# Kernel optimization log

Measured on AMD Instinct MI355X. Metric: run time of the kernel, lower is better.

## Reference

```python
import jax, jax.numpy as jnp
import numpy as np

N = 20000       # nodes
E = 320000      # edges (before self-loops)
F_IN = 1024     # num_features
H = 4           # head_num
C = 64          # hidden_size
NC = 4          # n_classes
NEG_SLOPE = 0.2 # PyG GATConv default


def setup_inputs() -> dict:
    key = jax.random.key(0)
    ks = jax.random.split(key, 16)
    def w(k, shape, fan_in):
        return jax.random.normal(k, shape, dtype=jnp.float32) / np.sqrt(fan_in)
    x = jax.random.normal(ks[0], (N, F_IN), dtype=jnp.float32)
    edge_index = jax.random.randint(ks[1], (2, E), 0, N, dtype=jnp.int64)
    return {
        "x": x,
        "edge_index": edge_index,
        # layer 1: F_IN -> H*C, concat
        "w1": w(ks[2], (F_IN, H * C), F_IN),
        "as1": w(ks[3], (H, C), C),
        "ad1": w(ks[4], (H, C), C),
        "b1": jnp.zeros((H * C,), jnp.float32),
        # layer 2: H*C -> H*C, concat
        "w2": w(ks[5], (H * C, H * C), H * C),
        "as2": w(ks[6], (H, C), C),
        "ad2": w(ks[7], (H, C), C),
        "b2": jnp.zeros((H * C,), jnp.float32),
        # out layer: H*C -> C, 1 head, concat=False
        "w3": w(ks[8], (H * C, 1 * C), H * C),
        "as3": w(ks[9], (1, C), C),
        "ad3": w(ks[10], (1, C), C),
        "b3": jnp.zeros((C,), jnp.float32),
        # classifier
        "wc": w(ks[11], (C, NC), C),
        "bc": jnp.zeros((NC,), jnp.float32),
    }


def gat_layer(x, src, dst, W, a_src, a_dst, bias, concat):
    """PyG GATConv (eval mode, self-loops already added to src/dst)."""
    n = x.shape[0]
    Hh, Cc = a_src.shape
    h = (x @ W).reshape(n, Hh, Cc)                       # [N,H,C]
    al_s = jnp.sum(h * a_src[None], axis=-1)             # [N,H]
    al_d = jnp.sum(h * a_dst[None], axis=-1)             # [N,H]
    e = al_s[src] + al_d[dst]                            # [E,H]
    e = jax.nn.leaky_relu(e, NEG_SLOPE)
    # segment softmax over incoming edges of each destination node
    emax = jax.ops.segment_max(e, dst, num_segments=n)   # [N,H]
    ex = jnp.exp(e - emax[dst])
    denom = jax.ops.segment_sum(ex, dst, num_segments=n) # [N,H]
    alpha = ex / (denom[dst] + 1e-16)                    # [E,H]
    msg = h[src] * alpha[..., None]                      # [E,H,C]
    out = jax.ops.segment_sum(msg, dst, num_segments=n)  # [N,H,C]
    if concat:
        out = out.reshape(n, Hh * Cc)
    else:
        out = out.mean(axis=1)
    return out + bias


def reference(x, edge_index, w1, as1, ad1, b1, w2, as2, ad2, b2,
              w3, as3, ad3, b3, wc, bc):
    n = x.shape[0]
    loop = jnp.arange(n, dtype=edge_index.dtype)
    src = jnp.concatenate([edge_index[0], loop])
    dst = jnp.concatenate([edge_index[1], loop])
    out = jax.nn.relu(gat_layer(x, src, dst, w1, as1, ad1, b1, True))
    out = jax.nn.relu(gat_layer(out, src, dst, w2, as2, ad2, b2, True))
    out = gat_layer(out, src, dst, w3, as3, ad3, b3, False)
    return out @ wc + bc                                  # [N, n_classes]
```

## Files before the change

### kernel.cpp

```cpp
#include <hip/hip_runtime.h>

#define N_NODES 20000
#define N_EDGES 320000
#define ET (N_EDGES + N_NODES)
#define F_IN 1024
#define HC 256
#define NC 4

typedef unsigned short ushort_t;
typedef __attribute__((ext_vector_type(8))) short short8;
typedef __attribute__((ext_vector_type(4))) float f32x4;

__device__ inline ushort_t f2bf(float f) {
    unsigned u = __float_as_uint(f);
    unsigned r = (u + 0x7fffu + ((u >> 16) & 1u)) >> 16;
    return (ushort_t)r;
}
__device__ inline float bf2f(ushort_t u) {
    return __uint_as_float(((unsigned)u) << 16);
}

__device__ inline unsigned cvt_pk_bf16(float lo, float hi) {
    unsigned r;
    asm("v_cvt_pk_bf16_f32 %0, %1, %2" : "=v"(r) : "v"(lo), "v"(hi));
    return r;
}

#define GLOAD16(gp, lp) __builtin_amdgcn_global_load_lds( \
    (const __attribute__((address_space(1))) void*)(gp),  \
    (__attribute__((address_space(3))) void*)(lp), 16, 0, 0)

__global__ void count_kernel(const int* __restrict__ ei, int* __restrict__ counts) {
    int e = blockIdx.x * blockDim.x + threadIdx.x;
    if (e >= ET) return;
    int dst = (e < N_EDGES) ? ei[N_EDGES + e] : (e - N_EDGES);
    atomicAdd(&counts[dst], 1);
}

__global__ void scan_kernel(const int* __restrict__ counts, int* __restrict__ row_ptr,
                            int* __restrict__ cursor) {
    __shared__ int sums[1024];
    int t = threadIdx.x;
    const int per = (N_NODES + 1023) / 1024;
    int b = t * per;
    int e = min(b + per, N_NODES);
    int s = 0;
    for (int i = b; i < e; ++i) s += counts[i];
    sums[t] = s;
    __syncthreads();
    for (int off = 1; off < 1024; off <<= 1) {
        int v = (t >= off) ? sums[t - off] : 0;
        __syncthreads();
        sums[t] += v;
        __syncthreads();
    }
    int run = (t == 0) ? 0 : sums[t - 1];
    for (int i = b; i < e; ++i) {
        row_ptr[i] = run;
        cursor[i]  = run;
        run += counts[i];
    }
    if (t == 0) row_ptr[N_NODES] = ET;
}

__global__ void scatter_kernel(const int* __restrict__ ei, int* __restrict__ cursor,
                               int* __restrict__ col) {
    int e = blockIdx.x * blockDim.x + threadIdx.x;
    if (e >= ET) return;
    int src, dst;
    if (e < N_EDGES) { src = ei[e]; dst = ei[N_EDGES + e]; }
    else             { src = dst = e - N_EDGES; }
    int pos = atomicAdd(&cursor[dst], 1);
    col[pos] = src;
}

__global__ void split_T(const float* __restrict__ in, ushort_t* __restrict__ hi,
                        ushort_t* __restrict__ lo, int K, int Nn) {
    int idx = blockIdx.x * blockDim.x + threadIdx.x;
    if (idx >= K * Nn) return;
    int k = idx / Nn, n = idx - k * Nn;
    float v = in[idx];
    ushort_t h = f2bf(v);
    hi[(size_t)n * K + k] = h;
    lo[(size_t)n * K + k] = f2bf(v - bf2f(h));
}

#define AL_EPILOGUE()                                                              \
    {                                                                              \
        float asv[NF], adv[NF];                                                    \
        _Pragma("unroll")                                                          \
        for (int j = 0; j < NF; ++j) {                                             \
            int col = bn + wn * SN + j * 16 + (lane & 15);                         \
            asv[j] = as_w[col];                                                    \
            adv[j] = ad_w[col];                                                    \
        }                                                                          \
        float* s_as = (float*)smem;                                   \
        float* s_ad = (float*)smem + 2 * BM;                                       \
        _Pragma("unroll")                                                          \
        for (int i = 0; i < MF; ++i) {                                             \
            _Pragma("unroll")                                                      \
            for (int rr = 0; rr < 4; ++rr) {                                       \
                float ps = 0.f, pd = 0.f;                                          \
                _Pragma("unroll")                                                  \
                for (int j = 0; j < NF; ++j) {                                     \
                    ps += acc[i][j][rr] * asv[j];                                  \
                    pd += acc[i][j][rr] * adv[j];                                  \
                }                                                                  \
                _Pragma("unroll")                                                  \
                for (int o = 1; o < 16; o <<= 1) {                                 \
                    ps += __shfl_xor(ps, o, 64);                                   \
                    pd += __shfl_xor(pd, o, 64);                                   \
                }                                                                  \
                if ((lane & 15) == 0) {                                            \
                    int rl = wm * SM + i * 16 + (lane >> 4) * 4 + rr;              \
                    s_as[wn * BM + rl] = ps;                                       \
                    s_ad[wn * BM + rl] = pd;                                       \
                }                                                                  \
            }                                                                      \
        }                                                                          \
        __syncthreads();                                                           \
        if (t < BM) {                                                              \
            int row = bm + t;                                                      \
            if (row < M) {                                                         \
                int hb = bn >> 6;                                                  \
                als[row * H + hb] = s_as[t] + s_as[BM + t];                        \
                ald[row * H + hb] = s_ad[t] + s_ad[BM + t];                        \
            }                                                                      \
        }                                                                          \
    }

template<int GY, int H>
__launch_bounds__(256)
__global__ void gemm_f32a(const float* __restrict__ X,
                          const ushort_t* __restrict__ BTh, const ushort_t* __restrict__ BTl,
                          float* __restrict__ C, const float* __restrict__ as_w,
                          const float* __restrict__ ad_w, float* __restrict__ als,
                          float* __restrict__ ald, int M, int K, int NT) {
    constexpr int BM = 128, BN = 64, SM = 64, SN = 32, MF = 4, NF = 2;
    __shared__ __align__(16) char smem[24576];
    char* Ash = smem;
    char* Asl = smem + 8192;
    char* Bsh = smem + 16384;
    char* Bsl = smem + 20480;

    const int t = threadIdx.x, lane = t & 63, w = t >> 6;
    const int wm = w >> 1, wn = w & 1;
    const int nwg = gridDim.x;
    const int id = blockIdx.x;
    const int q = nwg >> 3, r = nwg & 7;
    const int xcd = id & 7, idx = id >> 3;
    const int logical = (xcd < r ? xcd * (q + 1) : r * (q + 1) + (xcd - r) * q) + idx;
    const int bm = (logical / GY) * BM, bn = (logical % GY) * BN;

    const int achk = lane & 3;
    const float* xRow[2]; int aoff[2];
    #pragma unroll
    for (int qq = 0; qq < 2; ++qq) {
        int arow = (w * 2 + qq) * 16 + (lane >> 2);
        int grow = min(bm + arow, M - 1);
        xRow[qq] = X + (size_t)grow * K + achk * 8;
        aoff[qq] = arow * 64 + ((achk ^ ((arow >> 1) & 3)) * 16);
    }
    const int gchunk = ((lane & 3) ^ ((lane >> 3) & 3)) * 16;
    const int brow = w * 16 + (lane >> 2);
    const size_t gB = (size_t)(bn + brow) * K * 2 + gchunk;
    const int lB = w * 1024;

    const char* Bhb = (const char*)BTh;
    const char* Blb = (const char*)BTl;
    const int c16 = (lane >> 4);

    f32x4 acc[MF][NF];
    #pragma unroll
    for (int i = 0; i < MF; ++i)
        #pragma unroll
        for (int j = 0; j < NF; ++j) acc[i][j] = (f32x4){0.f, 0.f, 0.f, 0.f};

    float4 c0[2], c1[2];
    #pragma unroll
    for (int qq = 0; qq < 2; ++qq) {
        c0[qq] = *(const float4*)(xRow[qq]);
        c1[qq] = *(const float4*)(xRow[qq] + 4);
    }

    for (int k0 = 0; k0 < K; k0 += 32) {
        float4 n0[2], n1[2];
        if (k0 + 32 < K) {
            #pragma unroll
            for (int qq = 0; qq < 2; ++qq) {
                n0[qq] = *(const float4*)(xRow[qq] + k0 + 32);
                n1[qq] = *(const float4*)(xRow[qq] + k0 + 36);
            }
        }
        #pragma unroll
        for (int qq = 0; qq < 2; ++qq) {
            float vv[8] = {c0[qq].x, c0[qq].y, c0[qq].z, c0[qq].w,
                           c1[qq].x, c1[qq].y, c1[qq].z, c1[qq].w};
            unsigned hp[4], lp[4];
            #pragma unroll
            for (int j = 0; j < 4; ++j) {
                unsigned h = cvt_pk_bf16(vv[2 * j], vv[2 * j + 1]);
                float h0 = __uint_as_float(h << 16);
                float h1 = __uint_as_float(h & 0xFFFF0000u);
                hp[j] = h;
                lp[j] = cvt_pk_bf16(vv[2 * j] - h0, vv[2 * j + 1] - h1);
            }
            *(uint4*)(Ash + aoff[qq]) = make_uint4(hp[0], hp[1], hp[2], hp[3]);
            *(uint4*)(Asl + aoff[qq]) = make_uint4(lp[0], lp[1], lp[2], lp[3]);
        }
        size_t kb = (size_t)k0 * 2;
        GLOAD16(Bhb + gB + kb, Bsh + lB);
        GLOAD16(Blb + gB + kb, Bsl + lB);
        __syncthreads();
        short8 afh[MF], afl[MF], bfh[NF], bfl[NF];
        #pragma unroll
        for (int i = 0; i < MF; ++i) {
            int row = wm * SM + i * 16 + (lane & 15);
            int off = row * 64 + ((c16 ^ ((row >> 1) & 3)) * 16);
            afh[i] = *(const short8*)(Ash + off);
            afl[i] = *(const short8*)(Asl + off);
        }
        #pragma unroll
        for (int j = 0; j < NF; ++j) {
            int row = wn * SN + j * 16 + (lane & 15);
            int off = row * 64 + ((c16 ^ ((row >> 1) & 3)) * 16);
            bfh[j] = *(const short8*)(Bsh + off);
            bfl[j] = *(const short8*)(Bsl + off);
        }
        #pragma unroll
        for (int i = 0; i < MF; ++i)
            #pragma unroll
            for (int j = 0; j < NF; ++j) {
                acc[i][j] = __builtin_amdgcn_mfma_f32_16x16x32_bf16(afh[i], bfh[j], acc[i][j], 0, 0, 0);
                acc[i][j] = __builtin_amdgcn_mfma_f32_16x16x32_bf16(afh[i], bfl[j], acc[i][j], 0, 0, 0);
                acc[i][j] = __builtin_amdgcn_mfma_f32_16x16x32_bf16(afl[i], bfh[j], acc[i][j], 0, 0, 0);
            }
        __syncthreads();
        #pragma unroll
        for (int qq = 0; qq < 2; ++qq) { c0[qq] = n0[qq]; c1[qq] = n1[qq]; }
    }
    #pragma unroll
    for (int i = 0; i < MF; ++i) {
        int rbase = bm + wm * SM + i * 16 + (lane >> 4) * 4;
        #pragma unroll
        for (int j = 0; j < NF; ++j) {
            int col = bn + wn * SN + j * 16 + (lane & 15);
            #pragma unroll
            for (int rr = 0; rr < 4; ++rr)
                if (rbase + rr < M) C[(size_t)(rbase + rr) * NT + col] = acc[i][j][rr];
        }
    }
    AL_EPILOGUE()
}

template<int GY, int H>
__launch_bounds__(256)
__global__ void gemm_mfma(const ushort_t* __restrict__ Ah, const ushort_t* __restrict__ Al,
                          const ushort_t* __restrict__ BTh, const ushort_t* __restrict__ BTl,
                          float* __restrict__ C, const float* __restrict__ as_w,
                          const float* __restrict__ ad_w, float* __restrict__ als,
                          float* __restrict__ ald, int M, int K, int NT) {
    constexpr int BM = 128, BN = 64, SM = 64, SN = 32, MF = 4, NF = 2;
    __shared__ __align__(16) char smem[24576];
    char* Ash = smem;
    char* Asl = smem + 8192;
    char* Bsh = smem + 16384;
    char* Bsl = smem + 20480;

    const int t = threadIdx.x, lane = t & 63, w = t >> 6;
    const int wm = w >> 1, wn = w & 1;
    const int nwg = gridDim.x;
    const int id = blockIdx.x;
    const int q = nwg >> 3, r = nwg & 7;
    const int xcd = id & 7, idx = id >> 3;
    const int logical = (xcd < r ? xcd * (q + 1) : r * (q + 1) + (xcd - r) * q) + idx;
    const int bm = (logical / GY) * BM, bn = (logical % GY) * BN;
    const int gchunk = ((lane & 3) ^ ((lane >> 3) & 3)) * 16;

    size_t gA[2]; int lA[2];
    #pragma unroll
    for (int qq = 0; qq < 2; ++qq) {
        int arow = (w * 2 + qq) * 16 + (lane >> 2);
        int grow = min(bm + arow, M - 1);
        gA[qq] = (size_t)grow * K * 2 + gchunk;
        lA[qq] = (w * 2 + qq) * 1024;
    }
    const int brow = w * 16 + (lane >> 2);
    const size_t gB = (size_t)(bn + brow) * K * 2 + gchunk;
    const int lB = w * 1024;

    const char* Ahb = (const char*)Ah;
    const char* Alb = (const char*)Al;
    const char* Bhb = (const char*)BTh;
    const char* Blb = (const char*)BTl;
    const int c16 = (lane >> 4);

    f32x4 acc[MF][NF];
    #pragma unroll
    for (int i = 0; i < MF; ++i)
        #pragma unroll
        for (int j = 0; j < NF; ++j) acc[i][j] = (f32x4){0.f, 0.f, 0.f, 0.f};

    for (int k0 = 0; k0 < K; k0 += 32) {
        size_t kb = (size_t)k0 * 2;
        #pragma unroll
        for (int qq = 0; qq < 2; ++qq) {
            GLOAD16(Ahb + gA[qq] + kb, Ash + lA[qq]);
            GLOAD16(Alb + gA[qq] + kb, Asl + lA[qq]);
        }
        GLOAD16(Bhb + gB + kb, Bsh + lB);
        GLOAD16(Blb + gB + kb, Bsl + lB);
        __syncthreads();
        short8 afh[MF], afl[MF], bfh[NF], bfl[NF];
        #pragma unroll
        for (int i = 0; i < MF; ++i) {
            int row = wm * SM + i * 16 + (lane & 15);
            int off = row * 64 + ((c16 ^ ((row >> 1) & 3)) * 16);
            afh[i] = *(const short8*)(Ash + off);
            afl[i] = *(const short8*)(Asl + off);
        }
        #pragma unroll
        for (int j = 0; j < NF; ++j) {
            int row = wn * SN + j * 16 + (lane & 15);
            int off = row * 64 + ((c16 ^ ((row >> 1) & 3)) * 16);
            bfh[j] = *(const short8*)(Bsh + off);
            bfl[j] = *(const short8*)(Bsl + off);
        }
        #pragma unroll
        for (int i = 0; i < MF; ++i)
            #pragma unroll
            for (int j = 0; j < NF; ++j) {
                acc[i][j] = __builtin_amdgcn_mfma_f32_16x16x32_bf16(afh[i], bfh[j], acc[i][j], 0, 0, 0);
                acc[i][j] = __builtin_amdgcn_mfma_f32_16x16x32_bf16(afh[i], bfl[j], acc[i][j], 0, 0, 0);
                acc[i][j] = __builtin_amdgcn_mfma_f32_16x16x32_bf16(afl[i], bfh[j], acc[i][j], 0, 0, 0);
            }
        __syncthreads();
    }
    #pragma unroll
    for (int i = 0; i < MF; ++i) {
        int rbase = bm + wm * SM + i * 16 + (lane >> 4) * 4;
        #pragma unroll
        for (int j = 0; j < NF; ++j) {
            int col = bn + wn * SN + j * 16 + (lane & 15);
            #pragma unroll
            for (int rr = 0; rr < 4; ++rr)
                if (rbase + rr < M) C[(size_t)(rbase + rr) * NT + col] = acc[i][j][rr];
        }
    }
    AL_EPILOGUE()
}

template<int H>
__launch_bounds__(256)
__global__ void alpha_kernel(const float* __restrict__ als, const float* __restrict__ ald,
                             const int* __restrict__ row_ptr, const int* __restrict__ col,
                             float* __restrict__ alpha) {
    int lane = threadIdx.x & 63, w = threadIdx.x >> 6;
    int dst = blockIdx.x * 4 + w;
    if (dst >= N_NODES) return;
    int beg = row_ptr[dst], deg = row_ptr[dst + 1] - beg;
    constexpr int ES = 64 / H;
    int i_loc = lane / H, hh = lane % H;
    float ad = ald[dst * H + hh];
    float m = -1e30f, den = 0.f;
    for (int base = 0; base < deg; base += ES) {
        int i = base + i_loc;
        if (i < deg) {
            float e = als[col[beg + i] * H + hh] + ad;
            e = (e > 0.f) ? e : 0.2f * e;
            float nm = fmaxf(m, e);
            den = den * __expf(m - nm) + __expf(e - nm);
            m = nm;
        }
    }
    #pragma unroll
    for (int off = H; off < 64; off <<= 1) {
        float mo = __shfl_xor(m, off, 64);
        float dn = __shfl_xor(den, off, 64);
        float nm = fmaxf(m, mo);
        den = den * __expf(m - nm) + dn * __expf(mo - nm);
        m = nm;
    }
    float rden = 1.f / (den + 1e-16f);
    for (int base = 0; base < deg; base += ES) {
        int i = base + i_loc;
        if (i < deg) {
            float e = als[col[beg + i] * H + hh] + ad;
            e = (e > 0.f) ? e : 0.2f * e;
            alpha[(size_t)hh * ET + beg + i] = __expf(e - m) * rden;
        }
    }
}

template<int CT, int CW, int H, bool RELU, bool SPLIT>
__launch_bounds__(256)
__global__ void agg_v3(const float* __restrict__ h, const float* __restrict__ alpha,
                       const int* __restrict__ row_ptr, const int* __restrict__ col,
                       const float* __restrict__ bias,
                       ushort_t* __restrict__ oh, ushort_t* __restrict__ ol,
                       float* __restrict__ of) {
    constexpr int NS  = CT / CW;
    constexpr int LPT = CW / 4;
    constexpr int TPW = 64 / LPT;
    static_assert(NS == H, "slice==head mapping");
    __shared__ int   s_src[4][64];
    __shared__ float s_alp[4][64];
    const int nwg = gridDim.x;
    const int q = nwg >> 3;
    int id = blockIdx.x;
    int logical = (id & 7) * q + (id >> 3);
    int slice = logical / (N_NODES / 4);
    int g = logical - slice * (N_NODES / 4);
    int lane = threadIdx.x & 63, w = threadIdx.x >> 6;
    int dst = g * 4 + w;
    int beg = row_ptr[dst], deg = row_ptr[dst + 1] - beg;
    int team = lane / LPT;
    int cc = (lane & (LPT - 1)) * 4;

    const int*   colP = col + beg;
    const float* aP   = alpha + (size_t)slice * ET + beg;
    const float* hS   = h + slice * CW + cc;

    float4 acc = make_float4(0.f, 0.f, 0.f, 0.f);
    for (int base = 0; base < deg; base += 64) {
        int cnt = min(64, deg - base);
        if (lane < cnt) {
            s_src[w][lane] = colP[base + lane];
            s_alp[w][lane] = aP[base + lane];
        }
        for (int i = team; i < cnt; i += TPW) {
            int   s = s_src[w][i];
            float a = s_alp[w][i];
            float4 hv = *(const float4*)&hS[s * CT];
            acc.x += a * hv.x; acc.y += a * hv.y;
            acc.z += a * hv.z; acc.w += a * hv.w;
        }
    }
    #pragma unroll
    for (int off = LPT; off < 64; off <<= 1) {
        acc.x += __shfl_xor(acc.x, off, 64);
        acc.y += __shfl_xor(acc.y, off, 64);
        acc.z += __shfl_xor(acc.z, off, 64);
        acc.w += __shfl_xor(acc.w, off, 64);
    }
    if (team == 0) {
        int ch = slice * CW + cc;
        float4 bv = *(const float4*)&bias[ch];
        float v0 = acc.x + bv.x, v1 = acc.y + bv.y, v2 = acc.z + bv.z, v3 = acc.w + bv.w;
        if (RELU) {
            v0 = fmaxf(v0, 0.f); v1 = fmaxf(v1, 0.f);
            v2 = fmaxf(v2, 0.f); v3 = fmaxf(v3, 0.f);
        }
        size_t idx = (size_t)dst * CT + ch;
        if (SPLIT) {
            ushort4 h4, l4;
            h4.x = f2bf(v0); l4.x = f2bf(v0 - bf2f(h4.x));
            h4.y = f2bf(v1); l4.y = f2bf(v1 - bf2f(h4.y));
            h4.z = f2bf(v2); l4.z = f2bf(v2 - bf2f(h4.z));
            h4.w = f2bf(v3); l4.w = f2bf(v3 - bf2f(h4.w));
            *(ushort4*)&oh[idx] = h4;
            *(ushort4*)&ol[idx] = l4;
        } else {
            *(float4*)&of[idx] = make_float4(v0, v1, v2, v3);
        }
    }
}

__global__ void classifier_kernel(const float* __restrict__ x, const float* __restrict__ wc,
                                  const float* __restrict__ bc, float* __restrict__ out) {
    int n = blockIdx.x * blockDim.x + threadIdx.x;
    if (n >= N_NODES) return;
    float acc[NC] = {bc[0], bc[1], bc[2], bc[3]};
    for (int c = 0; c < 64; ++c) {
        float xv = x[(size_t)n * 64 + c];
        #pragma unroll
        for (int k = 0; k < NC; ++k) acc[k] += xv * wc[c * NC + k];
    }
    #pragma unroll
    for (int k = 0; k < NC; ++k) out[(size_t)n * NC + k] = acc[k];
}

extern "C" void kernel_launch(void* const* d_in, const int* in_sizes, int n_in,
                              void* d_out, int out_size, void* d_ws, size_t ws_size,
                              hipStream_t stream) {
    const float* x   = (const float*)d_in[0];
    const int*   ei  = (const int*)d_in[1];
    const float* w1  = (const float*)d_in[2];
    const float* as1 = (const float*)d_in[3];
    const float* ad1 = (const float*)d_in[4];
    const float* b1  = (const float*)d_in[5];
    const float* w2  = (const float*)d_in[6];
    const float* as2 = (const float*)d_in[7];
    const float* ad2 = (const float*)d_in[8];
    const float* b2  = (const float*)d_in[9];
    const float* w3  = (const float*)d_in[10];
    const float* as3 = (const float*)d_in[11];
    const float* ad3 = (const float*)d_in[12];
    const float* b3  = (const float*)d_in[13];
    const float* wc  = (const float*)d_in[14];
    const float* bc  = (const float*)d_in[15];
    float* out = (float*)d_out;

    char* ws = (char*)d_ws;
    size_t off = 0;
    auto alloc = [&](size_t bytes) -> char* {
        char* p = ws + off;
        off = (off + bytes + 255) & ~(size_t)255;
        return p;
    };

    int* counts  = (int*)alloc(N_NODES * 4);
    int* cursor  = (int*)alloc(N_NODES * 4);
    int* row_ptr = (int*)alloc((N_NODES + 1) * 4);
    int* colidx  = (int*)alloc(ET * 4);
    float* als   = (float*)alloc(N_NODES * 4 * 4);
    float* ald   = (float*)alloc(N_NODES * 4 * 4);
    float* alpha = (float*)alloc((size_t)4 * ET * 4);
    float* B0    = (float*)alloc((size_t)N_NODES * HC * 4);

    ushort_t* w1Th = (ushort_t*)alloc((size_t)F_IN * HC * 2);
    ushort_t* w1Tl = (ushort_t*)alloc((size_t)F_IN * HC * 2);
    ushort_t* w2Th = (ushort_t*)alloc((size_t)HC * HC * 2);
    ushort_t* w2Tl = (ushort_t*)alloc((size_t)HC * HC * 2);
    ushort_t* w3Th = (ushort_t*)alloc((size_t)HC * 64 * 2);
    ushort_t* w3Tl = (ushort_t*)alloc((size_t)HC * 64 * 2);
    ushort_t* B1h  = (ushort_t*)alloc((size_t)N_NODES * HC * 2);
    ushort_t* B1l  = (ushort_t*)alloc((size_t)N_NODES * HC * 2);
    float*    B1f  = (float*)alloc((size_t)N_NODES * 64 * 4);

    hipMemsetAsync(counts, 0, N_NODES * sizeof(int), stream);
    int eb = (ET + 255) / 256;
    count_kernel<<<eb, 256, 0, stream>>>(ei, counts);
    scan_kernel<<<1, 1024, 0, stream>>>(counts, row_ptr, cursor);
    scatter_kernel<<<eb, 256, 0, stream>>>(ei, cursor, colidx);

    split_T<<<(F_IN * HC + 255) / 256, 256, 0, stream>>>(w1, w1Th, w1Tl, F_IN, HC);
    split_T<<<(HC * HC + 255) / 256, 256, 0, stream>>>(w2, w2Th, w2Tl, HC, HC);
    split_T<<<(HC * 64 + 255) / 256, 256, 0, stream>>>(w3, w3Th, w3Tl, HC, 64);

    const int nwg128 = ((N_NODES + 127) / 128) * (HC / 64);
    const int nblk_dst = N_NODES / 4;
    gemm_f32a<4, 4><<<nwg128, 256, 0, stream>>>(x, w1Th, w1Tl, B0, as1, ad1, als, ald,
                                                N_NODES, F_IN, HC);
    alpha_kernel<4><<<nblk_dst, 256, 0, stream>>>(als, ald, row_ptr, colidx, alpha);
    agg_v3<256, 64, 4, true, true><<<4 * nblk_dst, 256, 0, stream>>>(
        B0, alpha, row_ptr, colidx, b1, B1h, B1l, nullptr);
    gemm_mfma<4, 4><<<nwg128, 256, 0, stream>>>(B1h, B1l, w2Th, w2Tl, B0, as2, ad2, als, ald,
                                                N_NODES, HC, HC);
    alpha_kernel<4><<<nblk_dst, 256, 0, stream>>>(als, ald, row_ptr, colidx, alpha);
    agg_v3<256, 64, 4, true, true><<<4 * nblk_dst, 256, 0, stream>>>(
        B0, alpha, row_ptr, colidx, b2, B1h, B1l, nullptr);
    const int nwg3 = (N_NODES + 127) / 128;
    gemm_mfma<1, 1><<<nwg3, 256, 0, stream>>>(B1h, B1l, w3Th, w3Tl, B0, as3, ad3, als, ald,
                                              N_NODES, HC, 64);
    alpha_kernel<1><<<nblk_dst, 256, 0, stream>>>(als, ald, row_ptr, colidx, alpha);
    agg_v3<64, 64, 1, false, false><<<nblk_dst, 256, 0, stream>>>(
        B0, alpha, row_ptr, colidx, b3, nullptr, nullptr, B1f);
    classifier_kernel<<<(N_NODES + 255) / 256, 256, 0, stream>>>(B1f, wc, bc, out);
}
```

Baseline: 298.9 us.

## Double K-step per barrier in GEMMs and shrink layer-3 tile to 64 rows

Both GEMM kernels now stage 64 K-elements per iteration (two 32-wide sub-tiles) before a single pair of barriers, halving the number of syncthreads per K sweep. The layer-3 GEMM is templated on BM and launched with 64-row tiles so more workgroups cover the 20000 rows. This doubles LDS use per block (48KB for the main GEMMs), which may reduce occupancy, and assumes K is a multiple of 64.

New measurement: 292.2 us. -2.2%, faster.

```diff
diff --git a/kernel.cpp b/kernel.cpp
--- a/kernel.cpp
+++ b/kernel.cpp
@@ -137,11 +137,7 @@
                           const float* __restrict__ ad_w, float* __restrict__ als,
                           float* __restrict__ ald, int M, int K, int NT) {
     constexpr int BM = 128, BN = 64, SM = 64, SN = 32, MF = 4, NF = 2;
-    __shared__ __align__(16) char smem[24576];
-    char* Ash = smem;
-    char* Asl = smem + 8192;
-    char* Bsh = smem + 16384;
-    char* Bsl = smem + 20480;
+    __shared__ __align__(16) char smem[49152];
 
     const int t = threadIdx.x, lane = t & 63, w = t >> 6;
     const int wm = w >> 1, wn = w & 1;
@@ -169,6 +165,7 @@
     const char* Bhb = (const char*)BTh;
     const char* Blb = (const char*)BTl;
     const int c16 = (lane >> 4);
+    const int NTs = K / 64;
 
     f32x4 acc[MF][NF];
     #pragma unroll
@@ -176,68 +173,81 @@
         #pragma unroll
         for (int j = 0; j < NF; ++j) acc[i][j] = (f32x4){0.f, 0.f, 0.f, 0.f};
 
-    float4 c0[2], c1[2];
-    #pragma unroll
-    for (int qq = 0; qq < 2; ++qq) {
-        c0[qq] = *(const float4*)(xRow[qq]);
-        c1[qq] = *(const float4*)(xRow[qq] + 4);
-    }
-
-    for (int k0 = 0; k0 < K; k0 += 32) {
-        float4 n0[2], n1[2];
-        if (k0 + 32 < K) {
-            #pragma unroll
-            for (int qq = 0; qq < 2; ++qq) {
-                n0[qq] = *(const float4*)(xRow[qq] + k0 + 32);
-                n1[qq] = *(const float4*)(xRow[qq] + k0 + 36);
-            }
-        }
-        #pragma unroll
-        for (int qq = 0; qq < 2; ++qq) {
-            float vv[8] = {c0[qq].x, c0[qq].y, c0[qq].z, c0[qq].w,
-                           c1[qq].x, c1[qq].y, c1[qq].z, c1[qq].w};
-            unsigned hp[4], lp[4];
-            #pragma unroll
-            for (int j = 0; j < 4; ++j) {
-                unsigned h = cvt_pk_bf16(vv[2 * j], vv[2 * j + 1]);
-                float h0 = __uint_as_float(h << 16);
-                float h1 = __uint_as_float(h & 0xFFFF0000u);
-                hp[j] = h;
-                lp[j] = cvt_pk_bf16(vv[2 * j] - h0, vv[2 * j + 1] - h1);
-            }
-            *(uint4*)(Ash + aoff[qq]) = make_uint4(hp[0], hp[1], hp[2], hp[3]);
-            *(uint4*)(Asl + aoff[qq]) = make_uint4(lp[0], lp[1], lp[2], lp[3]);
-        }
-        size_t kb = (size_t)k0 * 2;
-        GLOAD16(Bhb + gB + kb, Bsh + lB);
-        GLOAD16(Blb + gB + kb, Bsl + lB);
-        __syncthreads();
-        short8 afh[MF], afl[MF], bfh[NF], bfl[NF];
-        #pragma unroll
-        for (int i = 0; i < MF; ++i) {
-            int row = wm * SM + i * 16 + (lane & 15);
-            int off = row * 64 + ((c16 ^ ((row >> 1) & 3)) * 16);
-            afh[i] = *(const short8*)(Ash + off);
-            afl[i] = *(const short8*)(Asl + off);
-        }
-        #pragma unroll
-        for (int j = 0; j < NF; ++j) {
-            int row = wn * SN + j * 16 + (lane & 15);
-            int off = row * 64 + ((c16 ^ ((row >> 1) & 3)) * 16);
-            bfh[j] = *(const short8*)(Bsh + off);
-            bfl[j] = *(const short8*)(Bsl + off);
-        }
-        #pragma unroll
-        for (int i = 0; i < MF; ++i)
-            #pragma unroll
-            for (int j = 0; j < NF; ++j) {
-                acc[i][j] = __builtin_amdgcn_mfma_f32_16x16x32_bf16(afh[i], bfh[j], acc[i][j], 0, 0, 0);
-                acc[i][j] = __builtin_amdgcn_mfma_f32_16x16x32_bf16(afh[i], bfl[j], acc[i][j], 0, 0, 0);
-                acc[i][j] = __builtin_amdgcn_mfma_f32_16x16x32_bf16(afl[i], bfh[j], acc[i][j], 0, 0, 0);
+    float4 cur0[2][2], cur1[2][2], nxt0[2][2], nxt1[2][2];
+    #pragma unroll
+    for (int qq = 0; qq < 2; ++qq)
+        #pragma unroll
+        for (int kc = 0; kc < 2; ++kc) {
+            cur0[qq][kc] = *(const float4*)(xRow[qq] + kc * 32);
+            cur1[qq][kc] = *(const float4*)(xRow[qq] + kc * 32 + 4);
+        }
+
+    for (int ts = 0; ts < NTs; ++ts) {
+        size_t kb = (size_t)ts * 128;
+        #pragma unroll
+        for (int kc = 0; kc < 2; ++kc) {
+            GLOAD16(Bhb + gB + kb + kc * 64, smem + 32768 + kc * 4096 + lB);
+            GLOAD16(Blb + gB + kb + kc * 64, smem + 40960 + kc * 4096 + lB);
+        }
+        if (ts + 1 < NTs) {
+            #pragma unroll
+            for (int qq = 0; qq < 2; ++qq)
+                #pragma unroll
+                for (int kc = 0; kc < 2; ++kc) {
+                    nxt0[qq][kc] = *(const float4*)(xRow[qq] + (ts + 1) * 64 + kc * 32);
+                    nxt1[qq][kc] = *(const float4*)(xRow[qq] + (ts + 1) * 64 + kc * 32 + 4);
+                }
+        }
+        #pragma unroll
+        for (int qq = 0; qq < 2; ++qq)
+            #pragma unroll
+            for (int kc = 0; kc < 2; ++kc) {
+                float vv[8] = {cur0[qq][kc].x, cur0[qq][kc].y, cur0[qq][kc].z, cur0[qq][kc].w,
+                               cur1[qq][kc].x, cur1[qq][kc].y, cur1[qq][kc].z, cur1[qq][kc].w};
+                unsigned hp[4], lp[4];
+                #pragma unroll
+                for (int j = 0; j < 4; ++j) {
+                    unsigned h = cvt_pk_bf16(vv[2 * j], vv[2 * j + 1]);
+                    float h0 = __uint_as_float(h << 16);
+                    float h1 = __uint_as_float(h & 0xFFFF0000u);
+                    hp[j] = h;
+                    lp[j] = cvt_pk_bf16(vv[2 * j] - h0, vv[2 * j + 1] - h1);
+                }
+                *(uint4*)(smem + kc * 8192 + aoff[qq])         = make_uint4(hp[0], hp[1], hp[2], hp[3]);
+                *(uint4*)(smem + 16384 + kc * 8192 + aoff[qq]) = make_uint4(lp[0], lp[1], lp[2], lp[3]);
             }
         __syncthreads();
         #pragma unroll
-        for (int qq = 0; qq < 2; ++qq) { c0[qq] = n0[qq]; c1[qq] = n1[qq]; }
+        for (int kc = 0; kc < 2; ++kc) {
+            short8 afh[MF], afl[MF], bfh[NF], bfl[NF];
+            #pragma unroll
+            for (int i = 0; i < MF; ++i) {
+                int row = wm * SM + i * 16 + (lane & 15);
+                int off = row * 64 + ((c16 ^ ((row >> 1) & 3)) * 16);
+                afh[i] = *(const short8*)(smem + kc * 8192 + off);
+                afl[i] = *(const short8*)(smem + 16384 + kc * 8192 + off);
+            }
+            #pragma unroll
+            for (int j = 0; j < NF; ++j) {
+                int row = wn * SN + j * 16 + (lane & 15);
+                int off = row * 64 + ((c16 ^ ((row >> 1) & 3)) * 16);
+                bfh[j] = *(const short8*)(smem + 32768 + kc * 4096 + off);
+                bfl[j] = *(const short8*)(smem + 40960 + kc * 4096 + off);
+            }
+            #pragma unroll
+            for (int i = 0; i < MF; ++i)
+                #pragma unroll
+                for (int j = 0; j < NF; ++j) {
+                    acc[i][j] = __builtin_amdgcn_mfma_f32_16x16x32_bf16(afh[i], bfh[j], acc[i][j], 0, 0, 0);
+                    acc[i][j] = __builtin_amdgcn_mfma_f32_16x16x32_bf16(afh[i], bfl[j], acc[i][j], 0, 0, 0);
+                    acc[i][j] = __builtin_amdgcn_mfma_f32_16x16x32_bf16(afl[i], bfh[j], acc[i][j], 0, 0, 0);
+                }
+        }
+        __syncthreads();
+        #pragma unroll
+        for (int qq = 0; qq < 2; ++qq)
+            #pragma unroll
+            for (int kc = 0; kc < 2; ++kc) { cur0[qq][kc] = nxt0[qq][kc]; cur1[qq][kc] = nxt1[qq][kc]; }
     }
     #pragma unroll
     for (int i = 0; i < MF; ++i) {
@@ -253,19 +263,17 @@
     AL_EPILOGUE()
 }
 
-template<int GY, int H>
+template<int BMT, int GY, int H>
 __launch_bounds__(256)
 __global__ void gemm_mfma(const ushort_t* __restrict__ Ah, const ushort_t* __restrict__ Al,
                           const ushort_t* __restrict__ BTh, const ushort_t* __restrict__ BTl,
                           float* __restrict__ C, const float* __restrict__ as_w,
                           const float* __restrict__ ad_w, float* __restrict__ als,
                           float* __restrict__ ald, int M, int K, int NT) {
-    constexpr int BM = 128, BN = 64, SM = 64, SN = 32, MF = 4, NF = 2;
-    __shared__ __align__(16) char smem[24576];
-    char* Ash = smem;
-    char* Asl = smem + 8192;
-    char* Bsh = smem + 16384;
-    char* Bsl = smem + 20480;
+    constexpr int BM = BMT, BN = 64, SM = BM / 2, SN = 32, MF = SM / 16, NF = 2;
+    constexpr int AQ = BM / 64;
+    constexpr int ASZ = BM * 64;
+    __shared__ __align__(16) char smem[4 * ASZ + 16384];
 
     const int t = threadIdx.x, lane = t & 63, w = t >> 6;
     const int wm = w >> 1, wn = w & 1;
@@ -277,13 +285,14 @@
     const int bm = (logical / GY) * BM, bn = (logical % GY) * BN;
     const int gchunk = ((lane & 3) ^ ((lane >> 3) & 3)) * 16;
 
-    size_t gA[2]; int lA[2];
-    #pragma unroll
-    for (int qq = 0; qq < 2; ++qq) {
-        int arow = (w * 2 + qq) * 16 + (lane >> 2);
+    size_t gA[AQ]; int lA[AQ];
+    #pragma unroll
+    for (int qq = 0; qq < AQ; ++qq) {
+        int inst = w * AQ + qq;
+        int arow = inst * 16 + (lane >> 2);
         int grow = min(bm + arow, M - 1);
         gA[qq] = (size_t)grow * K * 2 + gchunk;
-        lA[qq] = (w * 2 + qq) * 1024;
+        lA[qq] = inst * 1024;
     }
     const int brow = w * 16 + (lane >> 2);
     const size_t gB = (size_t)(bn + brow) * K * 2 + gchunk;
@@ -294,6 +303,7 @@
     const char* Bhb = (const char*)BTh;
     const char* Blb = (const char*)BTl;
     const int c16 = (lane >> 4);
+    const int NTs = K / 64;
 
     f32x4 acc[MF][NF];
     #pragma unroll
@@ -301,39 +311,45 @@
         #pragma unroll
         for (int j = 0; j < NF; ++j) acc[i][j] = (f32x4){0.f, 0.f, 0.f, 0.f};
 
-    for (int k0 = 0; k0 < K; k0 += 32) {
-        size_t kb = (size_t)k0 * 2;
-        #pragma unroll
-        for (int qq = 0; qq < 2; ++qq) {
-            GLOAD16(Ahb + gA[qq] + kb, Ash + lA[qq]);
-            GLOAD16(Alb + gA[qq] + kb, Asl + lA[qq]);
-        }
-        GLOAD16(Bhb + gB + kb, Bsh + lB);
-        GLOAD16(Blb + gB + kb, Bsl + lB);
+    for (int ts = 0; ts < NTs; ++ts) {
+        size_t kb = (size_t)ts * 128;
+        #pragma unroll
+        for (int kc = 0; kc < 2; ++kc) {
+            #pragma unroll
+            for (int qq = 0; qq < AQ; ++qq) {
+                GLOAD16(Ahb + gA[qq] + kb + kc * 64, smem + kc * ASZ + lA[qq]);
+                GLOAD16(Alb + gA[qq] + kb + kc * 64, smem + 2 * ASZ + kc * ASZ + lA[qq]);
+            }
+            GLOAD16(Bhb + gB + kb + kc * 64, smem + 4 * ASZ + kc * 4096 + lB);
+            GLOAD16(Blb + gB + kb + kc * 64, smem + 4 * ASZ + 8192 + kc * 4096 + lB);
+        }
         __syncthreads();
-        short8 afh[MF], afl[MF], bfh[NF], bfl[NF];
-        #pragma unroll
-        for (int i = 0; i < MF; ++i) {
-            int row = wm * SM + i * 16 + (lane & 15);
-            int off = row * 64 + ((c16 ^ ((row >> 1) & 3)) * 16);
-            afh[i] = *(const short8*)(Ash + off);
-            afl[i] = *(const short8*)(Asl + off);
-        }
-        #pragma unroll
-        for (int j = 0; j < NF; ++j) {
-            int row = wn * SN + j * 16 + (lane & 15);
-            int off = row * 64 + ((c16 ^ ((row >> 1) & 3)) * 16);
-            bfh[j] = *(const short8*)(Bsh + off);
-            bfl[j] = *(const short8*)(Bsl + off);
-        }
-        #pragma unroll
-        for (int i = 0; i < MF; ++i)
+        #pragma unroll
+        for (int kc = 0; kc < 2; ++kc) {
+            short8 afh[MF], afl[MF], bfh[NF], bfl[NF];
+            #pragma unroll
+            for (int i = 0; i < MF; ++i) {
+                int row = wm * SM + i * 16 + (lane & 15);
+                int off = row * 64 + ((c16 ^ ((row >> 1) & 3)) * 16);
+                afh[i] = *(const short8*)(smem + kc * ASZ + off);
+                afl[i] = *(const short8*)(smem + 2 * ASZ + kc * ASZ + off);
+            }
             #pragma unroll
             for (int j = 0; j < NF; ++j) {
-                acc[i][j] = __builtin_amdgcn_mfma_f32_16x16x32_bf16(afh[i], bfh[j], acc[i][j], 0, 0, 0);
-                acc[i][j] = __builtin_amdgcn_mfma_f32_16x16x32_bf16(afh[i], bfl[j], acc[i][j], 0, 0, 0);
-                acc[i][j] = __builtin_amdgcn_mfma_f32_16x16x32_bf16(afl[i], bfh[j], acc[i][j], 0, 0, 0);
+                int row = wn * SN + j * 16 + (lane & 15);
+                int off = row * 64 + ((c16 ^ ((row >> 1) & 3)) * 16);
+                bfh[j] = *(const short8*)(smem + 4 * ASZ + kc * 4096 + off);
+                bfl[j] = *(const short8*)(smem + 4 * ASZ + 8192 + kc * 4096 + off);
             }
+            #pragma unroll
+            for (int i = 0; i < MF; ++i)
+                #pragma unroll
+                for (int j = 0; j < NF; ++j) {
+                    acc[i][j] = __builtin_amdgcn_mfma_f32_16x16x32_bf16(afh[i], bfh[j], acc[i][j], 0, 0, 0);
+                    acc[i][j] = __builtin_amdgcn_mfma_f32_16x16x32_bf16(afh[i], bfl[j], acc[i][j], 0, 0, 0);
+                    acc[i][j] = __builtin_amdgcn_mfma_f32_16x16x32_bf16(afl[i], bfh[j], acc[i][j], 0, 0, 0);
+                }
+        }
         __syncthreads();
     }
     #pragma unroll
@@ -545,14 +561,14 @@
     alpha_kernel<4><<<nblk_dst, 256, 0, stream>>>(als, ald, row_ptr, colidx, alpha);
     agg_v3<256, 64, 4, true, true><<<4 * nblk_dst, 256, 0, stream>>>(
         B0, alpha, row_ptr, colidx, b1, B1h, B1l, nullptr);
-    gemm_mfma<4, 4><<<nwg128, 256, 0, stream>>>(B1h, B1l, w2Th, w2Tl, B0, as2, ad2, als, ald,
-                                                N_NODES, HC, HC);
+    gemm_mfma<128, 4, 4><<<nwg128, 256, 0, stream>>>(B1h, B1l, w2Th, w2Tl, B0, as2, ad2,
+                                                     als, ald, N_NODES, HC, HC);
     alpha_kernel<4><<<nblk_dst, 256, 0, stream>>>(als, ald, row_ptr, colidx, alpha);
     agg_v3<256, 64, 4, true, true><<<4 * nblk_dst, 256, 0, stream>>>(
         B0, alpha, row_ptr, colidx, b2, B1h, B1l, nullptr);
-    const int nwg3 = (N_NODES + 127) / 128;
-    gemm_mfma<1, 1><<<nwg3, 256, 0, stream>>>(B1h, B1l, w3Th, w3Tl, B0, as3, ad3, als, ald,
-                                              N_NODES, HC, 64);
+    const int nwg3 = (N_NODES + 63) / 64;
+    gemm_mfma<64, 1, 1><<<nwg3, 256, 0, stream>>>(B1h, B1l, w3Th, w3Tl, B0, as3, ad3,
+                                                  als, ald, N_NODES, HC, 64);
     alpha_kernel<1><<<nblk_dst, 256, 0, stream>>>(als, ald, row_ptr, colidx, alpha);
     agg_v3<64, 64, 1, false, false><<<nblk_dst, 256, 0, stream>>>(
         B0, alpha, row_ptr, colidx, b3, nullptr, nullptr, B1f);
```
